# Optimization experiments

Hardware: AMD Instinct MI355X
Metric: run time of the kernel (lower is better)

Reference implementation:

```python
import jax, jax.numpy as jnp
import numpy as np

N = 50000
E = 800000
D_IN = 128
D_HID = 256
D_OUT = 128
BN_EPS = 1e-5


def setup_inputs() -> dict:
    key = jax.random.key(0)
    ks = jax.random.split(key, 12)
    v = jax.random.normal(ks[0], (N, D_IN), dtype=jnp.float32)
    edge_rows = jax.random.randint(ks[1], (E,), 0, N)
    edge_cols = jax.random.randint(ks[2], (E,), 0, N)
    edge_vals = jax.random.uniform(ks[3], (E,), dtype=jnp.float32)
    s1 = 1.0 / np.sqrt(D_IN)
    s2 = 1.0 / np.sqrt(D_HID)
    w1 = jax.random.uniform(ks[4], (D_IN, D_HID), minval=-s1, maxval=s1, dtype=jnp.float32)
    b1 = jax.random.uniform(ks[5], (D_HID,), minval=-s1, maxval=s1, dtype=jnp.float32)
    g1 = jnp.ones((D_HID,), dtype=jnp.float32)
    be1 = jnp.zeros((D_HID,), dtype=jnp.float32)
    w2 = jax.random.uniform(ks[6], (D_HID, D_OUT), minval=-s2, maxval=s2, dtype=jnp.float32)
    b2 = jax.random.uniform(ks[7], (D_OUT,), minval=-s2, maxval=s2, dtype=jnp.float32)
    g2 = jnp.ones((D_OUT,), dtype=jnp.float32)
    be2 = jnp.zeros((D_OUT,), dtype=jnp.float32)
    epsilon = jnp.zeros((1, 1), dtype=jnp.float32)  # nn.Parameter([[0.0]])
    return {"v": v, "edge_rows": edge_rows, "edge_cols": edge_cols,
            "edge_vals": edge_vals, "w1": w1, "b1": b1, "g1": g1, "be1": be1,
            "w2": w2, "b2": b2, "g2": g2, "be2": be2, "epsilon": epsilon}


def _batch_norm_relu(x, gamma, beta):
    # training-mode BatchNorm1d: batch stats over node axis, biased variance
    mean = jnp.mean(x, axis=0)
    var = jnp.var(x, axis=0)
    xhat = (x - mean) * jax.lax.rsqrt(var + BN_EPS)
    return jax.nn.relu(xhat * gamma + beta)


def reference(v, edge_rows, edge_cols, edge_vals, w1, b1, g1, be1, w2, b2, g2, be2, epsilon):
    # v_aggregate = sparse.mm(a, v): agg[r] += a[r,c] * v[c]
    msgs = edge_vals[:, None] * v[edge_cols]           # [E, D_IN]
    v_agg = jax.ops.segment_sum(msgs, edge_rows, num_segments=N)
    v_agg = v_agg + epsilon * v                         # epsilon residual ([[eps]] broadcasts)
    h = _batch_norm_relu(v_agg @ w1 + b1, g1, be1)      # Linear + BN + ReLU
    out = _batch_norm_relu(h @ w2 + b2, g2, be2)        # Linear + BN + ReLU
    return out
```

## Files before the change

kernel.cpp:

```cpp
#include <hip/hip_runtime.h>

#define D_IN 128
#define D_HID 256
#define D_OUT 128
#define BN_EPS 1e-5f

typedef unsigned short u16;
typedef unsigned int u32;
typedef __attribute__((ext_vector_type(8))) short bf16x8;
typedef __attribute__((ext_vector_type(4))) float f32x4;

__device__ __forceinline__ u16 f2b(float f) {
    u32 u = __float_as_uint(f);
    return (u16)((u + 0x7FFFu + ((u >> 16) & 1u)) >> 16);
}
__device__ __forceinline__ float b2f(u16 h) {
    return __uint_as_float(((u32)h) << 16);
}

__global__ __launch_bounds__(256) void cvt_w(
    const float* __restrict__ w1, const float* __restrict__ w2,
    u16* __restrict__ w1t, u16* __restrict__ w2t)
{
    int i = blockIdx.x * 256 + threadIdx.x;
    if (i < 32768) {
        int n = i >> 7, k = i & 127;
        w1t[i] = f2b(w1[k * 256 + n]);
    } else {
        int j = i - 32768;
        int n = j >> 8, k = j & 255;
        w2t[j] = f2b(w2[k * 128 + n]);
    }
}

__global__ __launch_bounds__(256) void cvt_v(
    const float* __restrict__ v, u16* __restrict__ vb, int total8)
{
    int i = blockIdx.x * 256 + threadIdx.x;
    if (i >= total8) return;
    float4 a = *reinterpret_cast<const float4*>(v + (size_t)i * 8);
    float4 b = *reinterpret_cast<const float4*>(v + (size_t)i * 8 + 4);
    u16 h[8] = {f2b(a.x), f2b(a.y), f2b(a.z), f2b(a.w),
                f2b(b.x), f2b(b.y), f2b(b.z), f2b(b.w)};
    *reinterpret_cast<uint4*>(vb + (size_t)i * 8) =
        *reinterpret_cast<uint4*>(h);
}

__global__ __launch_bounds__(256) void edge_hist(
    const int* __restrict__ rows, int* __restrict__ cnt, int E)
{
    int e = blockIdx.x * 256 + threadIdx.x;
    if (e < E) atomicAdd(&cnt[rows[e]], 1);
}

__global__ __launch_bounds__(256) void chunk_sums(
    const int* __restrict__ cnt, int* __restrict__ bsum, int N)
{
    __shared__ int red[256];
    const int t = threadIdx.x;
    const int i = blockIdx.x * 256 + t;
    red[t] = (i < N) ? cnt[i] : 0;
    __syncthreads();
#pragma unroll
    for (int off = 128; off > 0; off >>= 1) {
        if (t < off) red[t] += red[t + off];
        __syncthreads();
    }
    if (t == 0) bsum[blockIdx.x] = red[0];
}

__global__ __launch_bounds__(256) void scan_chunks(
    const int* __restrict__ bsum, int* __restrict__ coff, int NB)
{
    __shared__ int s[256];
    const int t = threadIdx.x;
    int c = (t < NB) ? bsum[t] : 0;
    s[t] = c;
    __syncthreads();
#pragma unroll
    for (int off = 1; off < 256; off <<= 1) {
        int x = (t >= off) ? s[t - off] : 0;
        __syncthreads();
        s[t] += x;
        __syncthreads();
    }
    coff[t] = s[t] - c;
}

__global__ __launch_bounds__(256) void scan_write(
    const int* __restrict__ cnt, const int* __restrict__ coff,
    int* __restrict__ rowstart, int* __restrict__ cursor, int N)
{
    __shared__ int s[256];
    const int t = threadIdx.x;
    const int i = blockIdx.x * 256 + t;
    int c = (i < N) ? cnt[i] : 0;
    s[t] = c;
    __syncthreads();
#pragma unroll
    for (int off = 1; off < 256; off <<= 1) {
        int x = (t >= off) ? s[t - off] : 0;
        __syncthreads();
        s[t] += x;
        __syncthreads();
    }
    int pos = coff[blockIdx.x] + s[t] - c;
    if (i < N) {
        rowstart[i] = pos;
        cursor[i] = pos;
    } else if (i == N) {
        rowstart[N] = pos;
    }
}

__global__ __launch_bounds__(256) void edge_scatter(
    const int* __restrict__ rows, const int* __restrict__ cols,
    const float* __restrict__ vals, int* __restrict__ cursor,
    float2* __restrict__ ecv, int E)
{
    int e = blockIdx.x * 256 + threadIdx.x;
    if (e >= E) return;
    int r = rows[e];
    int pos = atomicAdd(&cursor[r], 1);
    ecv[pos] = make_float2(__int_as_float(cols[e]), vals[e]);
}

__global__ __launch_bounds__(256) void spmm_rows(
    const u16* __restrict__ vb, const int* __restrict__ rowstart,
    const float2* __restrict__ ecv, const float* __restrict__ epsp,
    u16* __restrict__ x, int N)
{
    int wid = (blockIdx.x * 256 + threadIdx.x) >> 6;
    if (wid >= N) return;
    const int lane = threadIdx.x & 63;
    const int quarter = lane >> 4;
    const int l16 = lane & 15;
    const int s = rowstart[wid], e = rowstart[wid + 1];
    float acc[8] = {};

    for (int base = s; base < e; base += 64) {
        int n = min(64, e - base);
        float2 ev = make_float2(0.f, 0.f);
        if (base + lane < e) ev = ecv[base + lane];
        int mycol = __float_as_int(ev.x);
        int quads = (n + 3) >> 2;
        for (int k = 0; k < quads; ++k) {
            int idx = 4 * k + quarter;
            int col = __shfl(mycol, idx);
            float val = __shfl(ev.y, idx);
            uint4 vv = *reinterpret_cast<const uint4*>(
                vb + (size_t)col * D_IN + l16 * 8);
            const u16* hp = reinterpret_cast<const u16*>(&vv);
#pragma unroll
            for (int j = 0; j < 8; ++j)
                acc[j] = fmaf(val, b2f(hp[j]), acc[j]);
        }
    }
#pragma unroll
    for (int j = 0; j < 8; ++j) acc[j] += __shfl_down(acc[j], 32);
#pragma unroll
    for (int j = 0; j < 8; ++j) acc[j] += __shfl_down(acc[j], 16);
    if (quarter == 0) {
        const float eps = *epsp;
        uint4 vs = *reinterpret_cast<const uint4*>(
            vb + (size_t)wid * D_IN + l16 * 8);
        const u16* vp = reinterpret_cast<const u16*>(&vs);
        u16 o[8];
#pragma unroll
        for (int j = 0; j < 8; ++j)
            o[j] = f2b(fmaf(eps, b2f(vp[j]), acc[j]));
        *reinterpret_cast<uint4*>(x + (size_t)wid * D_IN + l16 * 8) =
            *reinterpret_cast<uint4*>(o);
    }
}

template <int KT, int NSTR, bool BNA>
__global__ __launch_bounds__(256) void gemm_mf(
    const u16* __restrict__ A, const u16* __restrict__ Bt,
    const float2* __restrict__ fA, u16* __restrict__ C,
    float* __restrict__ part1, float* __restrict__ part2, int M)
{
    __shared__ __align__(16) u16 As[64 * 128];
    __shared__ __align__(16) u16 Bs[128 * 128];
    __shared__ float2 fs[256];

    const int tid = threadIdx.x;
    const int bm = blockIdx.x * 64;
    const int bn0 = blockIdx.y * 128;
    const int l = tid & 63;
    const int wv = tid >> 6;
    const int wm = wv * 16;
    char* AsB = reinterpret_cast<char*>(As);
    char* BsB = reinterpret_cast<char*>(Bs);

    if (BNA) fs[tid] = fA[tid];

    f32x4 acc[8];
#pragma unroll
    for (int t = 0; t < 8; ++t) acc[t] = (f32x4){0.f, 0.f, 0.f, 0.f};

    for (int kk = 0; kk < KT; kk += 128) {
        __syncthreads();
#pragma unroll
        for (int i = 0; i < 4; ++i) {
            int c = tid + i * 256;
            int row = c >> 4, slot = c & 15;
            uint4 val = make_uint4(0u, 0u, 0u, 0u);
            if (bm + row < M)
                val = *reinterpret_cast<const uint4*>(
                    A + (size_t)(bm + row) * KT + kk + slot * 8);
            if (BNA) {
                u16* hp = reinterpret_cast<u16*>(&val);
#pragma unroll
                for (int j = 0; j < 8; ++j) {
                    float2 f = fs[kk + slot * 8 + j];
                    hp[j] = f2b(fmaxf(fmaf(b2f(hp[j]), f.x, f.y), 0.f));
                }
            }
            *reinterpret_cast<uint4*>(
                AsB + ((row * 256 + slot * 16) ^ ((row & 7) << 4))) = val;
        }
#pragma unroll
        for (int i = 0; i < 8; ++i) {
            int c = tid + i * 256;
            int n = c >> 4, slot = c & 15;
            uint4 val = *reinterpret_cast<const uint4*>(
                Bt + (size_t)(bn0 + n) * KT + kk + slot * 8);
            *reinterpret_cast<uint4*>(
                BsB + ((n * 256 + slot * 16) ^ ((n & 7) << 4))) = val;
        }
        __syncthreads();
#pragma unroll
        for (int s = 0; s < 4; ++s) {
            int ka = (s * 32 + (l >> 4) * 8) * 2;
            int arow = wm + (l & 15);
            bf16x8 af = *reinterpret_cast<bf16x8*>(
                AsB + ((arow * 256 + ka) ^ ((l & 7) << 4)));
#pragma unroll
            for (int t = 0; t < 8; ++t) {
                int brow = t * 16 + (l & 15);
                bf16x8 bfr = *reinterpret_cast<bf16x8*>(
                    BsB + ((brow * 256 + ka) ^ ((l & 7) << 4)));
                acc[t] = __builtin_amdgcn_mfma_f32_16x16x32_bf16(
                    af, bfr, acc[t], 0, 0, 0);
            }
        }
    }

    __syncthreads();

    float* bsF = reinterpret_cast<float*>(Bs);
#pragma unroll
    for (int t = 0; t < 8; ++t) {
        float s = acc[t][0] + acc[t][1] + acc[t][2] + acc[t][3];
        float q = acc[t][0] * acc[t][0] + acc[t][1] * acc[t][1]
                + acc[t][2] * acc[t][2] + acc[t][3] * acc[t][3];
        s += __shfl_down(s, 32);  q += __shfl_down(q, 32);
        s += __shfl_down(s, 16);  q += __shfl_down(q, 16);
        if (l < 16) {
            int c = t * 16 + l;
            bsF[wv * 128 + c]       = s;
            bsF[512 + wv * 128 + c] = q;
        }
    }

#pragma unroll
    for (int t = 0; t < 8; ++t) {
#pragma unroll
        for (int r = 0; r < 4; ++r) {
            int row = wm + (l >> 4) * 4 + r;
            int col = t * 16 + (l & 15);
            *reinterpret_cast<u16*>(
                AsB + ((row * 256 + col * 2) ^ ((row & 7) << 4))) =
                f2b(acc[t][r]);
        }
    }
    __syncthreads();

#pragma unroll
    for (int i = 0; i < 4; ++i) {
        int c = tid + i * 256;
        int row = c >> 4, slot = c & 15;
        if (bm + row < M) {
            uint4 val = *reinterpret_cast<uint4*>(
                AsB + ((row * 256 + slot * 16) ^ ((row & 7) << 4)));
            *reinterpret_cast<uint4*>(
                C + (size_t)(bm + row) * NSTR + bn0 + slot * 8) = val;
        }
    }
    if (tid < 128) {
        float s = bsF[tid] + bsF[128 + tid] + bsF[256 + tid] + bsF[384 + tid];
        float q = bsF[512 + tid] + bsF[640 + tid]
                + bsF[768 + tid] + bsF[896 + tid];
        part1[(size_t)blockIdx.x * NSTR + bn0 + tid] = s;
        part2[(size_t)blockIdx.x * NSTR + bn0 + tid] = q;
    }
}

__global__ void colreduce(const float* __restrict__ part1,
                          const float* __restrict__ part2,
                          float* __restrict__ sum, float* __restrict__ sq,
                          int NBX, int C)
{
    int col = threadIdx.x;
    float s = 0.f, q = 0.f;
    for (int bx = blockIdx.x; bx < NBX; bx += gridDim.x) {
        s += part1[(size_t)bx * C + col];
        q += part2[(size_t)bx * C + col];
    }
    atomicAdd(&sum[col], s);
    atomicAdd(&sq[col], q);
}

__global__ void bnfactors(const float* __restrict__ sum, const float* __restrict__ sq,
                          const float* __restrict__ g, const float* __restrict__ be,
                          float2* __restrict__ f, int C, int M)
{
    int c = threadIdx.x;
    if (c < C) {
        float inv = 1.f / (float)M;
        float mean = sum[c] * inv;
        float var = fmaxf(sq[c] * inv - mean * mean, 0.f);
        float s = g[c] * rsqrtf(var + BN_EPS);
        f[c] = make_float2(s, be[c] - mean * s);
    }
}

__global__ __launch_bounds__(256) void bnrelu_out(
    const u16* __restrict__ y2, const float2* __restrict__ f2,
    float* __restrict__ out, int total8)
{
    int i = blockIdx.x * 256 + threadIdx.x;
    if (i >= total8) return;
    uint4 val = *reinterpret_cast<const uint4*>(y2 + (size_t)i * 8);
    const u16* hp = reinterpret_cast<const u16*>(&val);
    int c = (i & 15) * 8;
    float r[8];
#pragma unroll
    for (int j = 0; j < 8; ++j) {
        float2 f = f2[c + j];
        r[j] = fmaxf(fmaf(b2f(hp[j]), f.x, f.y), 0.f);
    }
    *reinterpret_cast<float4*>(out + (size_t)i * 8) =
        make_float4(r[0], r[1], r[2], r[3]);
    *reinterpret_cast<float4*>(out + (size_t)i * 8 + 4) =
        make_float4(r[4], r[5], r[6], r[7]);
}

extern "C" void kernel_launch(void* const* d_in, const int* in_sizes, int n_in,
                              void* d_out, int out_size, void* d_ws, size_t ws_size,
                              hipStream_t stream)
{
    const float* v     = (const float*)d_in[0];
    const int*   erows = (const int*)d_in[1];
    const int*   ecols = (const int*)d_in[2];
    const float* evals = (const float*)d_in[3];
    const float* w1    = (const float*)d_in[4];
    const float* g1    = (const float*)d_in[6];
    const float* be1   = (const float*)d_in[7];
    const float* w2    = (const float*)d_in[8];
    const float* g2    = (const float*)d_in[10];
    const float* be2   = (const float*)d_in[11];
    const float* eps   = (const float*)d_in[12];

    const int M = in_sizes[0] / D_IN;
    const int E = in_sizes[3];
    const int NB = (M + 255) / 256;
    const int NBX = (M + 63) / 64;

    u16* xb  = (u16*)d_ws;
    u16* y1b = xb + (size_t)M * D_IN;
    u16* vb  = y1b + (size_t)M * D_HID;
    u16* w1t = vb + (size_t)M * D_IN;
    u16* w2t = w1t + 32768;
    int* rowstart = (int*)(w2t + 32768);
    int* cursor   = rowstart + M + 2;
    int* cnthist  = cursor + M;
    int* bsum     = cnthist + M;
    int* coff     = bsum + 256;
    size_t ecv_ofs = ((size_t)(coff + 256 - (int*)d_ws) + 1) & ~(size_t)1;
    float2* ecv = (float2*)((float*)d_ws + ecv_ofs);
    float* st   = (float*)(ecv + E);
    float* sum1 = st;
    float* sq1  = sum1 + D_HID;
    float* sum2 = sq1 + D_HID;
    float* sq2  = sum2 + D_OUT;
    float2* f1  = (float2*)(sq2 + D_OUT);
    float2* f2  = f1 + D_HID;
    float* pA1  = (float*)(f2 + D_OUT);
    float* pA2  = pA1 + (size_t)NBX * 256;
    float* pB1  = pA2 + (size_t)NBX * 256;
    float* pB2  = pB1 + (size_t)NBX * 128;
    u16* y2b    = xb;
    float* outp = (float*)d_out;

    hipMemsetAsync(cnthist, 0, (size_t)M * sizeof(int), stream);
    hipMemsetAsync(st, 0, (size_t)(2 * D_HID + 2 * D_OUT) * sizeof(float), stream);

    cvt_w<<<256, 256, 0, stream>>>(w1, w2, w1t, w2t);
    cvt_v<<<(M * D_IN / 8 + 255) / 256, 256, 0, stream>>>(v, vb, M * D_IN / 8);
    edge_hist<<<(E + 255) / 256, 256, 0, stream>>>(erows, cnthist, E);
    chunk_sums<<<NB, 256, 0, stream>>>(cnthist, bsum, M);
    scan_chunks<<<1, 256, 0, stream>>>(bsum, coff, NB);
    scan_write<<<NB, 256, 0, stream>>>(cnthist, coff, rowstart, cursor, M);
    edge_scatter<<<(E + 255) / 256, 256, 0, stream>>>(erows, ecols, evals, cursor, ecv, E);
    spmm_rows<<<(M * 64 + 255) / 256, 256, 0, stream>>>(vb, rowstart, ecv, eps, xb, M);

    dim3 grid1(NBX, 2);
    gemm_mf<128, 256, false><<<grid1, 256, 0, stream>>>(
        xb, w1t, nullptr, y1b, pA1, pA2, M);
    colreduce<<<16, 256, 0, stream>>>(pA1, pA2, sum1, sq1, NBX, 256);
    bnfactors<<<1, D_HID, 0, stream>>>(sum1, sq1, g1, be1, f1, D_HID, M);

    dim3 grid2(NBX, 1);
    gemm_mf<256, 128, true><<<grid2, 256, 0, stream>>>(
        y1b, w2t, f1, y2b, pB1, pB2, M);
    colreduce<<<16, 128, 0, stream>>>(pB1, pB2, sum2, sq2, NBX, 128);
    bnfactors<<<1, D_OUT, 0, stream>>>(sum2, sq2, g2, be2, f2, D_OUT, M);

    bnrelu_out<<<(M * D_OUT / 8 + 255) / 256, 256, 0, stream>>>(
        y2b, f2, outp, M * D_OUT / 8);
}
```

Measured before the change: 319.4 us.

## Split edge CSR scatter into coarse bucket pass and LDS fine pass

Replaces the single per-row global atomic scatter with two passes. A coarse pass bins edges into 64-row buckets using global atomics on bucket cursors and packs the local row index with the column into one 32-bit key. A per-bucket block then places each edge into its exact row slot using LDS atomics. This aims to localize the global writes and avoid scattered per-row atomics, at the cost of an extra pass over the edges and more workspace. The 16-bit column packing assumes column indices fit in 16 bits, but N=50000 does.

Measured after the change: 462.7 us. 44.8% more time.

```diff
diff --git a/kernel.cpp b/kernel.cpp
--- a/kernel.cpp
+++ b/kernel.cpp
@@ -4,6 +4,7 @@
 #define D_HID 256
 #define D_OUT 128
 #define BN_EPS 1e-5f
+#define RPB 64
 
 typedef unsigned short u16;
 typedef unsigned int u32;
@@ -89,7 +90,7 @@
 
 __global__ __launch_bounds__(256) void scan_write(
     const int* __restrict__ cnt, const int* __restrict__ coff,
-    int* __restrict__ rowstart, int* __restrict__ cursor, int N)
+    int* __restrict__ rowstart, int N)
 {
     __shared__ int s[256];
     const int t = threadIdx.x;
@@ -105,24 +106,52 @@
         __syncthreads();
     }
     int pos = coff[blockIdx.x] + s[t] - c;
-    if (i < N) {
-        rowstart[i] = pos;
-        cursor[i] = pos;
-    } else if (i == N) {
-        rowstart[N] = pos;
-    }
-}
-
-__global__ __launch_bounds__(256) void edge_scatter(
+    if (i < N) rowstart[i] = pos;
+    else if (i == N) rowstart[N] = pos;
+}
+
+__global__ __launch_bounds__(256) void bucket_init(
+    const int* __restrict__ rowstart, int* __restrict__ cursorB,
+    int NBUCK, int N)
+{
+    int b = blockIdx.x * 256 + threadIdx.x;
+    if (b < NBUCK) cursorB[b] = rowstart[min(b * RPB, N)];
+}
+
+__global__ __launch_bounds__(256) void scatter_coarse(
     const int* __restrict__ rows, const int* __restrict__ cols,
-    const float* __restrict__ vals, int* __restrict__ cursor,
-    float2* __restrict__ ecv, int E)
+    const float* __restrict__ vals, int* __restrict__ cursorB,
+    float2* __restrict__ ecv1, int E)
 {
     int e = blockIdx.x * 256 + threadIdx.x;
     if (e >= E) return;
     int r = rows[e];
-    int pos = atomicAdd(&cursor[r], 1);
-    ecv[pos] = make_float2(__int_as_float(cols[e]), vals[e]);
+    int pos = atomicAdd(&cursorB[r >> 6], 1);
+    u32 key = (u32)cols[e] | ((u32)(r & (RPB - 1)) << 16);
+    ecv1[pos] = make_float2(__uint_as_float(key), vals[e]);
+}
+
+__global__ __launch_bounds__(256) void scatter_fine(
+    const float2* __restrict__ ecv1, const int* __restrict__ rowstart,
+    float2* __restrict__ ecv, int N)
+{
+    __shared__ int cur[RPB];
+    const int b = blockIdx.x;
+    const int tid = threadIdx.x;
+    const int r0 = b * RPB;
+    const int nrows = min(RPB, N - r0);
+    if (tid < nrows) cur[tid] = rowstart[r0 + tid];
+    __syncthreads();
+    const int rs0 = rowstart[r0];
+    const int rs1 = rowstart[min(r0 + RPB, N)];
+    for (int e = rs0 + tid; e < rs1; e += 256) {
+        float2 p = ecv1[e];
+        u32 k = __float_as_uint(p.x);
+        int r6 = (int)(k >> 16);
+        int col = (int)(k & 0xFFFFu);
+        int pos = atomicAdd(&cur[r6], 1);
+        ecv[pos] = make_float2(__int_as_float(col), p.y);
+    }
 }
 
 __global__ __launch_bounds__(256) void spmm_rows(
@@ -367,6 +396,7 @@
     const int E = in_sizes[3];
     const int NB = (M + 255) / 256;
     const int NBX = (M + 63) / 64;
+    const int NBUCK = (M + RPB - 1) / RPB;
 
     u16* xb  = (u16*)d_ws;
     u16* y1b = xb + (size_t)M * D_IN;
@@ -374,13 +404,14 @@
     u16* w1t = vb + (size_t)M * D_IN;
     u16* w2t = w1t + 32768;
     int* rowstart = (int*)(w2t + 32768);
-    int* cursor   = rowstart + M + 2;
-    int* cnthist  = cursor + M;
+    int* cursorB  = rowstart + M + 2;
+    int* cnthist  = cursorB + NBUCK;
     int* bsum     = cnthist + M;
     int* coff     = bsum + 256;
     size_t ecv_ofs = ((size_t)(coff + 256 - (int*)d_ws) + 1) & ~(size_t)1;
-    float2* ecv = (float2*)((float*)d_ws + ecv_ofs);
-    float* st   = (float*)(ecv + E);
+    float2* ecv  = (float2*)((float*)d_ws + ecv_ofs);
+    float2* ecv1 = ecv + E;
+    float* st   = (float*)(ecv1 + E);
     float* sum1 = st;
     float* sq1  = sum1 + D_HID;
     float* sum2 = sq1 + D_HID;
@@ -402,8 +433,10 @@
     edge_hist<<<(E + 255) / 256, 256, 0, stream>>>(erows, cnthist, E);
     chunk_sums<<<NB, 256, 0, stream>>>(cnthist, bsum, M);
     scan_chunks<<<1, 256, 0, stream>>>(bsum, coff, NB);
-    scan_write<<<NB, 256, 0, stream>>>(cnthist, coff, rowstart, cursor, M);
-    edge_scatter<<<(E + 255) / 256, 256, 0, stream>>>(erows, ecols, evals, cursor, ecv, E);
+    scan_write<<<NB, 256, 0, stream>>>(cnthist, coff, rowstart, M);
+    bucket_init<<<(NBUCK + 255) / 256, 256, 0, stream>>>(rowstart, cursorB, NBUCK, M);
+    scatter_coarse<<<(E + 255) / 256, 256, 0, stream>>>(erows, ecols, evals, cursorB, ecv1, E);
+    scatter_fine<<<NBUCK, 256, 0, stream>>>(ecv1, rowstart, ecv, M);
     spmm_rows<<<(M * 64 + 255) / 256, 256, 0, stream>>>(vb, rowstart, ecv, eps, xb, M);
 
     dim3 grid1(NBX, 2);
```
